# Optimization experiments

Hardware: AMD Instinct MI355X
Metric: run time of the kernel (lower is better)

## Reference

```python
import jax, jax.numpy as jnp
import numpy as np

B, T, I, H, A = 128, 1024, 128, 256, 40


def setup_inputs() -> dict:
    key = jax.random.key(0)
    ks = jax.random.split(key, 10)
    s_ih = 1.0 / np.sqrt(H)
    return {
        "x": jax.random.normal(ks[0], (B, T, I), dtype=jnp.float32),
        "W_ih": jax.random.uniform(ks[1], (3 * H, I), minval=-s_ih, maxval=s_ih, dtype=jnp.float32),
        "W_hh": jax.random.uniform(ks[2], (3 * H, H), minval=-s_ih, maxval=s_ih, dtype=jnp.float32),
        "b_ih": jax.random.uniform(ks[3], (3 * H,), minval=-s_ih, maxval=s_ih, dtype=jnp.float32),
        "b_hh": jax.random.uniform(ks[4], (3 * H,), minval=-s_ih, maxval=s_ih, dtype=jnp.float32),
        "wv_W": jax.random.normal(ks[5], (A, H), dtype=jnp.float32) * 0.05,
        "wv_b": jnp.zeros((A,), dtype=jnp.float32),
        "wu": jax.random.uniform(ks[6], (A,), dtype=jnp.float32),
        "h2o_W": jax.random.normal(ks[7], (1, H), dtype=jnp.float32) * 0.05,
        "h2o_b": jnp.zeros((1,), dtype=jnp.float32),
    }


def _gru_outputs(x, W_ih, W_hh, b_ih, b_hh):
    # Precompute input-side gate projections for all timesteps: [B,T,3H]
    gx = jnp.einsum("bti,gi->btg", x, W_ih) + b_ih
    h0 = jnp.zeros((x.shape[0], H), dtype=x.dtype)

    def step(h, gx_t):
        gh = h @ W_hh.T + b_hh                      # [B,3H]
        xr, xz, xn = jnp.split(gx_t, 3, axis=-1)    # torch gate order r,z,n
        hr, hz, hn = jnp.split(gh, 3, axis=-1)
        r = jax.nn.sigmoid(xr + hr)
        z = jax.nn.sigmoid(xz + hz)
        n = jnp.tanh(xn + r * hn)
        h_new = (1.0 - z) * n + z * h
        return h_new, h_new

    _, hs = jax.lax.scan(step, h0, jnp.swapaxes(gx, 0, 1))  # hs: [T,B,H]
    return jnp.swapaxes(hs, 0, 1)  # [B,T,H]


def reference(x, W_ih, W_hh, b_ih, b_hh, wv_W, wv_b, wu, h2o_W, h2o_b):
    outputs = _gru_outputs(x, W_ih, W_hh, b_ih, b_hh)          # [B,T,H]
    um = jnp.tanh(jnp.einsum("bth,ah->bta", outputs, wv_W) + wv_b)  # [B,T,A]
    alpha = jax.nn.softmax(um @ wu, axis=1)                    # [B,T]
    context = jnp.einsum("bt,bth->bh", alpha, outputs)         # [B,H]
    # dropout_layer is identity in eval mode
    out = context @ h2o_W.T + h2o_b                            # [B,1]
    return out
```

## Files before the change

kernel.cpp:

```cpp
#include <hip/hip_runtime.h>


#define B_ 128
#define T_ 1024
#define I_ 128
#define H_ 256
#define G_ 768
#define A_ 40

typedef _Float16 f16;
typedef _Float16 f16x2 __attribute__((ext_vector_type(2)));

__device__ __forceinline__ float fdot2(unsigned a, unsigned b, float c){
#if __has_builtin(__builtin_amdgcn_fdot2)
  return __builtin_amdgcn_fdot2(__builtin_bit_cast(f16x2, a),
                                __builtin_bit_cast(f16x2, b), c, false);
#else
  f16x2 av = __builtin_bit_cast(f16x2, a), bv = __builtin_bit_cast(f16x2, b);
  return c + (float)av.x * (float)bv.x + (float)av.y * (float)bv.y;
#endif
}

__device__ __forceinline__ float2 h2f(unsigned u){
  f16x2 h = __builtin_bit_cast(f16x2, u);
  return make_float2((float)h.x, (float)h.y);
}
__device__ __forceinline__ unsigned f2h2(float a, float b){
  f16x2 h; h.x = (f16)a; h.y = (f16)b;
  return __builtin_bit_cast(unsigned, h);
}
__device__ __forceinline__ float sigm_(float x){ return 1.f / (1.f + __expf(-x)); }
__device__ __forceinline__ float tanh_(float x){ return 1.f - 2.f / (__expf(2.f * x) + 1.f); }

__global__ __launch_bounds__(256) void k_prep_w(const float* __restrict__ W,
                                                unsigned* __restrict__ Wp){
  int idx = blockIdx.x * 256 + threadIdx.x;
  int r = idx >> 7;
  int d = idx & 127;
  Wp[(size_t)d * G_ + r] = f2h2(W[r * 256 + 2 * d], W[r * 256 + 2 * d + 1]);
}

__global__ __launch_bounds__(256) void k_gx(const float* __restrict__ x,
                                            const float* __restrict__ wih,
                                            const float* __restrict__ bih,
                                            unsigned* __restrict__ gx){
  __shared__ __align__(16) unsigned Au[32 * 68];
  __shared__ __align__(16) unsigned Bu[32 * 68];
  const int tid = threadIdx.x;
  const int m0 = blockIdx.x * 64, n0 = blockIdx.y * 64;
  const int ar = tid >> 4, bc = tid & 15;
  float acc[4][4] = {{0.f}};

  for (int kh = 0; kh < 2; ++kh){
    __syncthreads();
    #pragma unroll
    for (int u = 0; u < 4; ++u){
      int idx = tid + 256 * u;
      int row = idx >> 4;
      int kq  = idx & 15;
      float4 va = *(const float4*)(x   + (size_t)(m0 + row) * I_ + kh * 64 + kq * 4);
      float4 vb = *(const float4*)(wih + (size_t)(n0 + row) * I_ + kh * 64 + kq * 4);
      Au[(2*kq  ) * 68 + row] = f2h2(va.x, va.y);
      Au[(2*kq+1) * 68 + row] = f2h2(va.z, va.w);
      Bu[(2*kq  ) * 68 + row] = f2h2(vb.x, vb.y);
      Bu[(2*kq+1) * 68 + row] = f2h2(vb.z, vb.w);
    }
    __syncthreads();
    #pragma unroll 8
    for (int kp = 0; kp < 32; ++kp){
      uint4 a4 = *(const uint4*)(Au + kp * 68 + ar * 4);
      uint4 b4 = *(const uint4*)(Bu + kp * 68 + bc * 4);
      acc[0][0]=fdot2(a4.x,b4.x,acc[0][0]); acc[0][1]=fdot2(a4.x,b4.y,acc[0][1]);
      acc[0][2]=fdot2(a4.x,b4.z,acc[0][2]); acc[0][3]=fdot2(a4.x,b4.w,acc[0][3]);
      acc[1][0]=fdot2(a4.y,b4.x,acc[1][0]); acc[1][1]=fdot2(a4.y,b4.y,acc[1][1]);
      acc[1][2]=fdot2(a4.y,b4.z,acc[1][2]); acc[1][3]=fdot2(a4.y,b4.w,acc[1][3]);
      acc[2][0]=fdot2(a4.z,b4.x,acc[2][0]); acc[2][1]=fdot2(a4.z,b4.y,acc[2][1]);
      acc[2][2]=fdot2(a4.z,b4.z,acc[2][2]); acc[2][3]=fdot2(a4.z,b4.w,acc[2][3]);
      acc[3][0]=fdot2(a4.w,b4.x,acc[3][0]); acc[3][1]=fdot2(a4.w,b4.y,acc[3][1]);
      acc[3][2]=fdot2(a4.w,b4.z,acc[3][2]); acc[3][3]=fdot2(a4.w,b4.w,acc[3][3]);
    }
  }

  float bn[4];
  #pragma unroll
  for (int j = 0; j < 4; ++j) bn[j] = bih[n0 + bc * 4 + j];
  #pragma unroll
  for (int i = 0; i < 4; ++i){
    int m = m0 + ar * 4 + i;
    uint2 st;
    st.x = f2h2(acc[i][0] + bn[0], acc[i][1] + bn[1]);
    st.y = f2h2(acc[i][2] + bn[2], acc[i][3] + bn[3]);
    *(uint2*)(gx + (size_t)m * (G_ / 2) + n0 / 2 + bc * 2) = st;
  }
}

__global__ __launch_bounds__(768, 3) void k_gru(const unsigned* __restrict__ Wp,
                                                unsigned* __restrict__ gx,
                                                const float* __restrict__ bhh){
  __shared__ uint4 Hc4[32];
  __shared__ float GH[512];
  const int tid = threadIdx.x;
  const int b = blockIdx.x;

  unsigned w[128];
  #pragma unroll
  for (int d = 0; d < 128; ++d) w[d] = Wp[(size_t)d * G_ + tid];

  const float bias = bhh[tid];
  float hprev = 0.f;
  if (tid < 32) Hc4[tid] = make_uint4(0, 0, 0, 0);

  f16* gxp = (f16*)gx + (size_t)b * T_ * G_;

  float xcur  = (float)gxp[tid];
  float xncur = (tid < 256) ? (float)gxp[512 + tid] : 0.f;
  __syncthreads();

  for (int t = 0; t < T_; ++t){
    float xnext = 0.f, xnnext = 0.f;
    if (t + 1 < T_){
      xnext = (float)gxp[(size_t)(t + 1) * G_ + tid];
      if (tid < 256) xnnext = (float)gxp[(size_t)(t + 1) * G_ + 512 + tid];
    }

    float a0 = 0.f, a1 = 0.f;
    #pragma unroll
    for (int j = 0; j < 32; ++j){
      uint4 hv = Hc4[j];
      a0 = fdot2(w[4*j+0], hv.x, a0); a1 = fdot2(w[4*j+1], hv.y, a1);
      a0 = fdot2(w[4*j+2], hv.z, a0); a1 = fdot2(w[4*j+3], hv.w, a1);
    }
    float a = a0 + a1;

    if (tid >= 512)      GH[tid - 256] = a + bias;
    else if (tid >= 256) GH[tid - 256] = sigm_(a + bias + xcur);
    __syncthreads();

    if (tid < 256){
      float rg = sigm_(xcur + a + bias);
      float zg = GH[tid];
      float ng = tanh_(xncur + rg * GH[256 + tid]);
      float h  = (1.f - zg) * ng + zg * hprev;
      hprev = h;
      f16 hh = (f16)h;
      ((f16*)Hc4)[tid] = hh;
      gxp[(size_t)t * G_ + tid] = hh;
      xncur = xnnext;
    }
    xcur = xnext;
    __syncthreads();
  }
}

__global__ __launch_bounds__(256) void k_score(const f16* __restrict__ outs,
                                               const float* __restrict__ wvW,
                                               const float* __restrict__ wvb,
                                               const float* __restrict__ wu,
                                               float* __restrict__ s){
  __shared__ uint4 OT[32 * 33];
  __shared__ float WV[A_ * 260];
  const int tid = threadIdx.x;
  const int m0 = blockIdx.x * 32;

  #pragma unroll
  for (int u = 0; u < 4; ++u){
    int idx = tid + 256 * u;
    int row = idx >> 5, col = idx & 31;
    OT[row * 33 + col] = *(const uint4*)(outs + (size_t)(m0 + row) * G_ + col * 8);
  }
  #pragma unroll
  for (int u = 0; u < 10; ++u){
    int f = tid + 256 * u;
    int a = f >> 6, k4 = f & 63;
    float4 v = *(const float4*)(wvW + a * 256 + k4 * 4);
    *(float4*)(WV + a * 260 + k4 * 4) = v;
  }
  __syncthreads();

  const int m = tid >> 3, aq = tid & 7;
  float acc[5] = {0.f, 0.f, 0.f, 0.f, 0.f};
  for (int i = 0; i < 32; ++i){
    uint4 oc = OT[m * 33 + i];
    float2 o01 = h2f(oc.x), o23 = h2f(oc.y), o45 = h2f(oc.z), o67 = h2f(oc.w);
    #pragma unroll
    for (int sa = 0; sa < 5; ++sa){
      int a = aq + sa * 8;
      const float* wr = &WV[a * 260 + i * 8];
      float4 w0 = *(const float4*)wr;
      float4 w1 = *(const float4*)(wr + 4);
      acc[sa] += o01.x*w0.x + o01.y*w0.y + o23.x*w0.z + o23.y*w0.w
               + o45.x*w1.x + o45.y*w1.y + o67.x*w1.z + o67.y*w1.w;
    }
  }
  float sp = 0.f;
  #pragma unroll
  for (int sa = 0; sa < 5; ++sa){
    int a = aq + sa * 8;
    sp += wu[a] * tanh_(acc[sa] + wvb[a]);
  }
  sp += __shfl_xor(sp, 1);
  sp += __shfl_xor(sp, 2);
  sp += __shfl_xor(sp, 4);
  if (aq == 0) s[m0 + m] = sp;
}

__global__ __launch_bounds__(256) void k_ctx(const f16* __restrict__ outs,
                                             const float* __restrict__ s,
                                             const float* __restrict__ h2oW,
                                             const float* __restrict__ h2ob,
                                             float* __restrict__ out){
  __shared__ float AL[T_];
  __shared__ float red[8];
  const int tid = threadIdx.x;
  const int b = blockIdx.x;
  const float* sb = s + (size_t)b * T_;

  float v0 = sb[tid], v1 = sb[tid + 256], v2 = sb[tid + 512], v3 = sb[tid + 768];
  float mx = fmaxf(fmaxf(v0, v1), fmaxf(v2, v3));
  #pragma unroll
  for (int msk = 1; msk < 64; msk <<= 1) mx = fmaxf(mx, __shfl_xor(mx, msk));
  if ((tid & 63) == 0) red[tid >> 6] = mx;
  __syncthreads();
  mx = fmaxf(fmaxf(red[0], red[1]), fmaxf(red[2], red[3]));

  float e0 = __expf(v0 - mx), e1 = __expf(v1 - mx), e2 = __expf(v2 - mx), e3 = __expf(v3 - mx);
  float zs = e0 + e1 + e2 + e3;
  #pragma unroll
  for (int msk = 1; msk < 64; msk <<= 1) zs += __shfl_xor(zs, msk);
  if ((tid & 63) == 0) red[4 + (tid >> 6)] = zs;
  __syncthreads();
  float invZ = 1.f / (red[4] + red[5] + red[6] + red[7]);
  AL[tid] = e0 * invZ; AL[tid + 256] = e1 * invZ;
  AL[tid + 512] = e2 * invZ; AL[tid + 768] = e3 * invZ;
  __syncthreads();

  const f16* ob = outs + (size_t)b * T_ * G_;
  float acc = 0.f;
  for (int t = 0; t < T_; t += 4){
    acc += AL[t + 0] * (float)ob[(size_t)(t + 0) * G_ + tid];
    acc += AL[t + 1] * (float)ob[(size_t)(t + 1) * G_ + tid];
    acc += AL[t + 2] * (float)ob[(size_t)(t + 2) * G_ + tid];
    acc += AL[t + 3] * (float)ob[(size_t)(t + 3) * G_ + tid];
  }
  __syncthreads();
  float val = acc * h2oW[tid];
  #pragma unroll
  for (int msk = 1; msk < 64; msk <<= 1) val += __shfl_xor(val, msk);
  if ((tid & 63) == 0) red[tid >> 6] = val;
  __syncthreads();
  if (tid == 0) out[b] = red[0] + red[1] + red[2] + red[3] + h2ob[0];
}

extern "C" void kernel_launch(void* const* d_in, const int* in_sizes, int n_in,
                              void* d_out, int out_size, void* d_ws, size_t ws_size,
                              hipStream_t stream){
  const float* x    = (const float*)d_in[0];
  const float* wih  = (const float*)d_in[1];
  const float* whh  = (const float*)d_in[2];
  const float* bih  = (const float*)d_in[3];
  const float* bhh  = (const float*)d_in[4];
  const float* wvW  = (const float*)d_in[5];
  const float* wvb  = (const float*)d_in[6];
  const float* wu   = (const float*)d_in[7];
  const float* h2oW = (const float*)d_in[8];
  const float* h2ob = (const float*)d_in[9];
  float* out = (float*)d_out;

  char* ws = (char*)d_ws;
  float*    s  = (float*)ws;
  unsigned* Wp = (unsigned*)(ws + 524288);
  unsigned* gx = (unsigned*)(ws + 917504);

  k_prep_w<<<384, 256, 0, stream>>>(whh, Wp);
  k_gx<<<dim3((B_ * T_) / 64, G_ / 64), 256, 0, stream>>>(x, wih, bih, gx);
  k_gru<<<B_, 768, 0, stream>>>(Wp, gx, bhh);
  k_score<<<(B_ * T_) / 32, 256, 0, stream>>>((const f16*)gx, wvW, wvb, wu, s);
  k_ctx<<<B_, 256, 0, stream>>>((const f16*)gx, s, h2oW, h2ob, out);
}
```

Baseline: 1.636 ms.

## Batch GRU recurrence over 16 sequences per block using MFMA

The recurrent step now processes 16 batch rows per block and computes the hidden projection with 16x16x32 f16 MFMA instructions, keeping W_hh fragments in registers and double-buffering the hidden state in shared memory so each step needs one barrier. The r and z recurrent biases are folded into the input projection, and W_hh is pre-swizzled into MFMA fragment order. This replaces per-sequence dot2 loops over 128 blocks with matrix-core work on only 8 blocks, which reduces parallelism across the GPU in exchange for much higher per-block throughput on the serial recurrence.

```diff
diff --git a/kernel.cpp b/kernel.cpp
--- a/kernel.cpp
+++ b/kernel.cpp
@@ -10,6 +10,9 @@
 
 typedef _Float16 f16;
 typedef _Float16 f16x2 __attribute__((ext_vector_type(2)));
+typedef _Float16 f16x4 __attribute__((ext_vector_type(4)));
+typedef _Float16 f16x8 __attribute__((ext_vector_type(8)));
+typedef float    f32x4 __attribute__((ext_vector_type(4)));
 
 __device__ __forceinline__ float fdot2(unsigned a, unsigned b, float c){
 #if __has_builtin(__builtin_amdgcn_fdot2)
@@ -34,15 +37,20 @@
 
 __global__ __launch_bounds__(256) void k_prep_w(const float* __restrict__ W,
                                                 unsigned* __restrict__ Wp){
-  int idx = blockIdx.x * 256 + threadIdx.x;
-  int r = idx >> 7;
-  int d = idx & 127;
-  Wp[(size_t)d * G_ + r] = f2h2(W[r * 256 + 2 * d], W[r * 256 + 2 * d + 1]);
+  int u = blockIdx.x * 256 + threadIdx.x;
+  int i2 = u & 3;
+  int l  = (u >> 2) & 63;
+  int kt = (u >> 8) & 7;
+  int nt = u >> 11;
+  int n = nt * 16 + (l & 15);
+  int k = kt * 32 + (l >> 4) * 8 + i2 * 2;
+  Wp[u] = f2h2(W[n * 256 + k], W[n * 256 + k + 1]);
 }
 
 __global__ __launch_bounds__(256) void k_gx(const float* __restrict__ x,
                                             const float* __restrict__ wih,
                                             const float* __restrict__ bih,
+                                            const float* __restrict__ bhh,
                                             unsigned* __restrict__ gx){
   __shared__ __align__(16) unsigned Au[32 * 68];
   __shared__ __align__(16) unsigned Bu[32 * 68];
@@ -83,7 +91,10 @@
 
   float bn[4];
   #pragma unroll
-  for (int j = 0; j < 4; ++j) bn[j] = bih[n0 + bc * 4 + j];
+  for (int j = 0; j < 4; ++j){
+    int n = n0 + bc * 4 + j;
+    bn[j] = bih[n] + (n < 512 ? bhh[n] : 0.f);
+  }
   #pragma unroll
   for (int i = 0; i < 4; ++i){
     int m = m0 + ar * 4 + i;
@@ -94,61 +105,100 @@
   }
 }
 
-__global__ __launch_bounds__(768, 3) void k_gru(const unsigned* __restrict__ Wp,
+__global__ __launch_bounds__(512, 1) void k_gru(const uint4* __restrict__ Wp4,
                                                 unsigned* __restrict__ gx,
                                                 const float* __restrict__ bhh){
-  __shared__ uint4 Hc4[32];
-  __shared__ float GH[512];
+  __shared__ uint4 hbuf[2][512];
   const int tid = threadIdx.x;
-  const int b = blockIdx.x;
-
-  unsigned w[128];
-  #pragma unroll
-  for (int d = 0; d < 128; ++d) w[d] = Wp[(size_t)d * G_ + tid];
-
-  const float bias = bhh[tid];
-  float hprev = 0.f;
-  if (tid < 32) Hc4[tid] = make_uint4(0, 0, 0, 0);
-
-  f16* gxp = (f16*)gx + (size_t)b * T_ * G_;
-
-  float xcur  = (float)gxp[tid];
-  float xncur = (tid < 256) ? (float)gxp[512 + tid] : 0.f;
-  __syncthreads();
-
+  const int w = tid >> 6, l = tid & 63;
+  const int q = l >> 4, m = l & 15;
+  const int b0 = blockIdx.x * 16;
+  const int cb0 = 32 * w + 4 * q;
+
+  uint4 Wf[6][8];
+  const int ntb[6] = {2*w, 2*w+1, 16+2*w, 17+2*w, 32+2*w, 33+2*w};
+  #pragma unroll
+  for (int tt = 0; tt < 6; ++tt)
+    #pragma unroll
+    for (int kt = 0; kt < 8; ++kt)
+      Wf[tt][kt] = Wp4[(ntb[tt] * 8 + kt) * 64 + l];
+
+  float bn0[4], bn1[4];
+  #pragma unroll
+  for (int j = 0; j < 4; ++j){
+    bn0[j] = bhh[512 + cb0 + j];
+    bn1[j] = bhh[512 + cb0 + 16 + j];
+  }
+
+  f16* gxw = (f16*)gx;
+  const size_t rbase = (size_t)(b0 + m) * T_;
+
+  const f16* x0 = gxw + rbase * G_;
+  uint2 xr0 = *(const uint2*)(x0 + cb0),       xr1 = *(const uint2*)(x0 + cb0 + 16);
+  uint2 xz0 = *(const uint2*)(x0 + 256 + cb0), xz1 = *(const uint2*)(x0 + 256 + cb0 + 16);
+  uint2 xn0 = *(const uint2*)(x0 + 512 + cb0), xn1 = *(const uint2*)(x0 + 512 + cb0 + 16);
+
+  hbuf[0][tid] = make_uint4(0, 0, 0, 0);
+  float hprev[2][4] = {{0.f}};
+  __syncthreads();
+
+  int cur = 0;
   for (int t = 0; t < T_; ++t){
-    float xnext = 0.f, xnnext = 0.f;
+    uint2 pr0, pz0, pn0, pr1, pz1, pn1;
     if (t + 1 < T_){
-      xnext = (float)gxp[(size_t)(t + 1) * G_ + tid];
-      if (tid < 256) xnnext = (float)gxp[(size_t)(t + 1) * G_ + 512 + tid];
-    }
-
-    float a0 = 0.f, a1 = 0.f;
-    #pragma unroll
-    for (int j = 0; j < 32; ++j){
-      uint4 hv = Hc4[j];
-      a0 = fdot2(w[4*j+0], hv.x, a0); a1 = fdot2(w[4*j+1], hv.y, a1);
-      a0 = fdot2(w[4*j+2], hv.z, a0); a1 = fdot2(w[4*j+3], hv.w, a1);
-    }
-    float a = a0 + a1;
-
-    if (tid >= 512)      GH[tid - 256] = a + bias;
-    else if (tid >= 256) GH[tid - 256] = sigm_(a + bias + xcur);
+      const f16* nx = gxw + (rbase + t + 1) * G_;
+      pr0 = *(const uint2*)(nx + cb0);       pr1 = *(const uint2*)(nx + cb0 + 16);
+      pz0 = *(const uint2*)(nx + 256 + cb0); pz1 = *(const uint2*)(nx + 256 + cb0 + 16);
+      pn0 = *(const uint2*)(nx + 512 + cb0); pn1 = *(const uint2*)(nx + 512 + cb0 + 16);
+    } else {
+      pr0=pz0=pn0=pr1=pz1=pn1=make_uint2(0,0);
+    }
+
+    uint4 bf[8];
+    #pragma unroll
+    for (int kt = 0; kt < 8; ++kt)
+      bf[kt] = hbuf[cur][(4 * kt + q) * 16 + m];
+
+    f32x4 acc[6];
+    #pragma unroll
+    for (int tt = 0; tt < 6; ++tt) acc[tt] = (f32x4){0.f, 0.f, 0.f, 0.f};
+    #pragma unroll
+    for (int kt = 0; kt < 8; ++kt){
+      f16x8 bv = __builtin_bit_cast(f16x8, bf[kt]);
+      #pragma unroll
+      for (int tt = 0; tt < 6; ++tt)
+        acc[tt] = __builtin_amdgcn_mfma_f32_16x16x32_f16(
+            __builtin_bit_cast(f16x8, Wf[tt][kt]), bv, acc[tt], 0, 0, 0);
+    }
+
+    uint2* hnext2 = (uint2*)hbuf[cur ^ 1];
+    f16*   orow   = gxw + (rbase + t) * G_;
+    #pragma unroll
+    for (int p = 0; p < 2; ++p){
+      f16x4 xrv = __builtin_bit_cast(f16x4, p ? xr1 : xr0);
+      f16x4 xzv = __builtin_bit_cast(f16x4, p ? xz1 : xz0);
+      f16x4 xnv = __builtin_bit_cast(f16x4, p ? xn1 : xn0);
+      const float* bnv = p ? bn1 : bn0;
+      f32x4 aR = acc[0 + p], aZ = acc[2 + p], aN = acc[4 + p];
+      float hh[4];
+      #pragma unroll
+      for (int j = 0; j < 4; ++j){
+        float r  = sigm_((float)xrv[j] + aR[j]);
+        float zg = sigm_((float)xzv[j] + aZ[j]);
+        float n  = tanh_((float)xnv[j] + r * (aN[j] + bnv[j]));
+        float h  = (1.f - zg) * n + zg * hprev[p][j];
+        hprev[p][j] = h;
+        hh[j] = h;
+      }
+      unsigned u0 = f2h2(hh[0], hh[1]), u1 = f2h2(hh[2], hh[3]);
+      hnext2[((4*w + 2*p + (q >> 1)) * 16 + m) * 2 + (q & 1)] = make_uint2(u0, u1);
+      *(uint2*)(orow + cb0 + 16 * p) = make_uint2(u0, u1);
+    }
+
     __syncthreads();
-
-    if (tid < 256){
-      float rg = sigm_(xcur + a + bias);
-      float zg = GH[tid];
-      float ng = tanh_(xncur + rg * GH[256 + tid]);
-      float h  = (1.f - zg) * ng + zg * hprev;
-      hprev = h;
-      f16 hh = (f16)h;
-      ((f16*)Hc4)[tid] = hh;
-      gxp[(size_t)t * G_ + tid] = hh;
-      xncur = xnnext;
-    }
-    xcur = xnext;
-    __syncthreads();
+    cur ^= 1;
+    xr0 = pr0; xz0 = pz0; xn0 = pn0;
+    xr1 = pr1; xz1 = pz1; xn1 = pn1;
   }
 }
 
@@ -272,8 +322,8 @@
   unsigned* gx = (unsigned*)(ws + 917504);
 
   k_prep_w<<<384, 256, 0, stream>>>(whh, Wp);
-  k_gx<<<dim3((B_ * T_) / 64, G_ / 64), 256, 0, stream>>>(x, wih, bih, gx);
-  k_gru<<<B_, 768, 0, stream>>>(Wp, gx, bhh);
+  k_gx<<<dim3((B_ * T_) / 64, G_ / 64), 256, 0, stream>>>(x, wih, bih, bhh, gx);
+  k_gru<<<8, 512, 0, stream>>>((const uint4*)Wp, gx, bhh);
   k_score<<<(B_ * T_) / 32, 256, 0, stream>>>((const f16*)gx, wvW, wvb, wu, s);
   k_ctx<<<B_, 256, 0, stream>>>((const f16*)gx, s, h2oW, h2ob, out);
 }
```

New measurement: 3.560 ms. 2.18x slower.
